# Performance work log

Measured on AMD Instinct MI355X. Metric: run time of the kernel, lower is better.

The kernel has to match this reference:

```python
import jax, jax.numpy as jnp
import numpy as np


def _log_g(x):
    # log of g(x) = where(x>=0, x+0.5, sigmoid(x)), computed stably in log-space
    return jnp.where(x >= 0, jnp.log(jax.nn.relu(x) + 0.5), -jax.nn.softplus(-x))


def _mingru_layer(h, w_hg_l, w_out_l, rms_w_l):
    # h: [B,T,H]; w_hg_l: [2*DI,H]; w_out_l: [H,DI]; rms_w_l: [H]
    hg = jnp.einsum('bth,dh->btd', h, w_hg_l)          # [B,T,2*DI]
    hidden, gate = jnp.split(hg, 2, axis=-1)            # each [B,T,DI]
    log_coeffs = -jax.nn.softplus(gate)                 # log a_t
    log_values = -jax.nn.softplus(-gate) + _log_g(hidden)  # log(z_t * g(h~_t))
    # Heinsen log-space associative scan (prev_hidden = 0, contributes nothing)
    a_star = jnp.cumsum(log_coeffs, axis=1)
    log_h = a_star + jax.lax.cumlogsumexp(log_values - a_star, axis=1)
    out = jnp.exp(log_h)                                # [B,T,DI]
    out = jnp.einsum('btd,hd->bth', out, w_out_l) + h   # proj_out + residual
    eps = jnp.finfo(out.dtype).eps
    out = out * jax.lax.rsqrt(jnp.mean(out * out, axis=-1, keepdims=True) + eps)
    return out * rms_w_l


def setup_inputs() -> dict:
    key = jax.random.key(0)
    ks = jax.random.split(key, 6)
    B, T, OBS, H, DI, L, A = 32, 1024, 512, 512, 1024, 2, 16
    s = 0.05  # weight scale keeps softplus/exp chain well-conditioned
    return {
        'x': jax.random.normal(ks[0], (B, T, OBS), jnp.float32),
        'enc_w': s * jax.random.normal(ks[1], (H, OBS), jnp.float32),
        'enc_b': jnp.zeros((H,), jnp.float32),
        'w_hg': s * jax.random.normal(ks[2], (L, 2 * DI, H), jnp.float32),
        'w_out': s * jax.random.normal(ks[3], (L, H, DI), jnp.float32),
        'rms_w': jnp.ones((L, H), jnp.float32),
        'dec_w': s * jax.random.normal(ks[4], (A, H), jnp.float32),
        'dec_b': jnp.zeros((A,), jnp.float32),
        'val_w': s * jax.random.normal(ks[5], (1, H), jnp.float32),
        'val_b': jnp.zeros((1,), jnp.float32),
    }


def reference(x, enc_w, enc_b, w_hg, w_out, rms_w, dec_w, dec_b, val_w, val_b):
    B, T, _ = x.shape
    # encoder: Linear + exact gelu
    h = jax.nn.gelu(jnp.einsum('bto,ho->bth', x, enc_w) + enc_b, approximate=False)
    for l in range(w_hg.shape[0]):
        h = _mingru_layer(h, w_hg[l], w_out[l], rms_w[l])
    flat = h.reshape(B * T, -1)
    logits = flat @ dec_w.T + dec_b                     # [B*T, A]
    values = (flat @ val_w.T + val_b).reshape(B, T)
    return logits, values
```

## Files before the change

kernel.cpp:

```cpp
#include <hip/hip_runtime.h>
#include <math.h>

#define MROWS 32768
#define T_LEN 1024

typedef __attribute__((ext_vector_type(8))) short bf16x8;
typedef __attribute__((ext_vector_type(4))) float f32x4;

__device__ __forceinline__ unsigned short f2bf(float f) {
  union { float f; unsigned u; } x; x.f = f;
  unsigned r = x.u + 0x7fffu + ((x.u >> 16) & 1u);
  return (unsigned short)(r >> 16);
}
__device__ __forceinline__ float bf2f(unsigned short u) {
  union { unsigned u; float f; } x; x.u = ((unsigned)u) << 16; return x.f;
}

__device__ __forceinline__ void gload_lds16(const void* g, void* l) {
  __builtin_amdgcn_global_load_lds(
      (const __attribute__((address_space(1))) void*)g,
      (__attribute__((address_space(3))) void*)l, 16, 0, 0);
}

template<int MODE>
__global__ __launch_bounds__(256, 2)
void gemm_bt(const unsigned short* __restrict__ A, int lda,
             const unsigned short* __restrict__ B,
             int N, int K,
             const float* __restrict__ bias,
             const unsigned short* res,
             unsigned short* outb)
{
  __shared__ __align__(16) unsigned short sA[128 * 64];
  __shared__ __align__(16) unsigned short sB[128 * 64];
  const int tid  = threadIdx.x;
  const int wave = tid >> 6, lane = tid & 63;
  const int m0 = blockIdx.x * 128, n0 = blockIdx.y * 128;
  const int srow   = lane >> 3;
  const int sslotb = ((lane & 7) ^ srow) * 16;
  const int wm = wave & 1, wn = wave >> 1;
  const int r16 = lane & 15, q = lane >> 4;

  f32x4 acc[4][4];
#pragma unroll
  for (int i = 0; i < 4; i++)
#pragma unroll
    for (int j = 0; j < 4; j++)
#pragma unroll
      for (int e = 0; e < 4; e++) acc[i][j][e] = 0.0f;

  const char* Ab = (const char*)A;
  const char* Bb = (const char*)B;
  char* sAb = (char*)sA;
  char* sBb = (char*)sB;

  for (int kt = 0; kt < K; kt += 64) {
#pragma unroll
    for (int i = 0; i < 4; i++) {
      const int j = wave * 4 + i;
      const int row = j * 8 + srow;
      gload_lds16(Ab + ((size_t)(m0 + row) * lda + kt) * 2 + sslotb, sAb + j * 1024);
      gload_lds16(Bb + ((size_t)(n0 + row) * K   + kt) * 2 + sslotb, sBb + j * 1024);
    }
    __syncthreads();
#pragma unroll
    for (int kh = 0; kh < 2; kh++) {
      bf16x8 af[4], bfr[4];
#pragma unroll
      for (int mt = 0; mt < 4; mt++) {
        const int row = wm * 64 + mt * 16 + r16;
        af[mt] = *(const bf16x8*)(sAb + row * 128 + ((((kh << 2) | q) ^ (row & 7)) * 16));
      }
#pragma unroll
      for (int nt = 0; nt < 4; nt++) {
        const int row = wn * 64 + nt * 16 + r16;
        bfr[nt] = *(const bf16x8*)(sBb + row * 128 + ((((kh << 2) | q) ^ (row & 7)) * 16));
      }
#pragma unroll
      for (int mt = 0; mt < 4; mt++)
#pragma unroll
        for (int nt = 0; nt < 4; nt++)
          acc[mt][nt] = __builtin_amdgcn_mfma_f32_16x16x32_bf16(af[mt], bfr[nt], acc[mt][nt], 0, 0, 0);
    }
    __syncthreads();
  }

#pragma unroll
  for (int mt = 0; mt < 4; mt++) {
#pragma unroll
    for (int nt = 0; nt < 4; nt++) {
#pragma unroll
      for (int r = 0; r < 4; r++) {
        const int m = m0 + wm * 64 + mt * 16 + q * 4 + r;
        const int n = n0 + wn * 64 + nt * 16 + r16;
        const size_t idx = (size_t)m * N + n;
        float v = acc[mt][nt][r];
        if (MODE == 0) {
          v += bias[n];
          v = 0.5f * v * (1.0f + erff(v * 0.70710678118654752f));
        } else if (MODE == 2) {
          v += bf2f(res[idx]);
        }
        outb[idx] = f2bf(v);
      }
    }
  }
}

__global__ __launch_bounds__(1024)
void scan_kernel(unsigned short* hg) {
  __shared__ float sA[32 * 64];
  __shared__ float sH[32 * 64];
  __shared__ float sC[32 * 64];
  const int b  = blockIdx.x >> 4;
  const int dg = blockIdx.x & 15;
  const int tid = threadIdx.x;
  const int c  = tid >> 5;
  const int dl = tid & 31;
  unsigned int* base = (unsigned int*)(hg + (size_t)b * T_LEN * 2048);
  const int du = dg * 32 + dl;

  float A0 = 1.0f, A1 = 1.0f, h0 = 0.0f, h1 = 0.0f;
#pragma unroll 8
  for (int tl = 0; tl < 32; ++tl) {
    const int t = c * 32 + tl;
    const unsigned hidp = base[t * 1024 + du];
    const unsigned gtp  = base[t * 1024 + 512 + du];
    const float hid0 = bf2f((unsigned short)hidp), hid1 = bf2f((unsigned short)(hidp >> 16));
    const float gt0  = bf2f((unsigned short)gtp),  gt1  = bf2f((unsigned short)(gtp >> 16));
    const float z0 = 1.0f / (1.0f + __expf(-gt0));
    const float z1 = 1.0f / (1.0f + __expf(-gt1));
    const float g0 = (hid0 >= 0.0f) ? (hid0 + 0.5f) : (1.0f / (1.0f + __expf(-hid0)));
    const float g1 = (hid1 >= 0.0f) ? (hid1 + 0.5f) : (1.0f / (1.0f + __expf(-hid1)));
    const unsigned short ra0 = f2bf(1.0f - z0), rb0 = f2bf(z0 * g0);
    const unsigned short ra1 = f2bf(1.0f - z1), rb1 = f2bf(z1 * g1);
    base[t * 1024 + du]       = (unsigned)ra0 | ((unsigned)ra1 << 16);
    base[t * 1024 + 512 + du] = (unsigned)rb0 | ((unsigned)rb1 << 16);
    const float fa0 = bf2f(ra0), fb0 = bf2f(rb0), fa1 = bf2f(ra1), fb1 = bf2f(rb1);
    A0 *= fa0; h0 = fa0 * h0 + fb0;
    A1 *= fa1; h1 = fa1 * h1 + fb1;
  }
  sA[c * 64 + 2 * dl] = A0;  sA[c * 64 + 2 * dl + 1] = A1;
  sH[c * 64 + 2 * dl] = h0;  sH[c * 64 + 2 * dl + 1] = h1;
  __syncthreads();

  if (tid < 64) {
    float hin = 0.0f;
#pragma unroll
    for (int cc = 0; cc < 32; ++cc) {
      sC[cc * 64 + tid] = hin;
      hin = sH[cc * 64 + tid] + sA[cc * 64 + tid] * hin;
    }
  }
  __syncthreads();

  float hh0 = sC[c * 64 + 2 * dl];
  float hh1 = sC[c * 64 + 2 * dl + 1];
#pragma unroll 8
  for (int tl = 0; tl < 32; ++tl) {
    const int t = c * 32 + tl;
    const unsigned pa = base[t * 1024 + du];
    const unsigned pb = base[t * 1024 + 512 + du];
    const float fa0 = bf2f((unsigned short)pa), fa1 = bf2f((unsigned short)(pa >> 16));
    const float fb0 = bf2f((unsigned short)pb), fb1 = bf2f((unsigned short)(pb >> 16));
    hh0 = fa0 * hh0 + fb0;
    hh1 = fa1 * hh1 + fb1;
    base[t * 1024 + 512 + du] = (unsigned)f2bf(hh0) | ((unsigned)f2bf(hh1) << 16);
  }
}

__global__ __launch_bounds__(256)
void rms_kernel(unsigned short* __restrict__ hb, const float* __restrict__ w) {
  const int wid  = (blockIdx.x * blockDim.x + threadIdx.x) >> 6;
  const int lane = threadIdx.x & 63;
  unsigned short* row = hb + (size_t)wid * 512;
  float v[8];
  float ss = 0.0f;
#pragma unroll
  for (int j = 0; j < 8; j++) { v[j] = bf2f(row[lane + 64 * j]); ss += v[j] * v[j]; }
#pragma unroll
  for (int off = 32; off >= 1; off >>= 1) ss += __shfl_xor(ss, off, 64);
  const float r = rsqrtf(ss * (1.0f / 512.0f) + 1.1920929e-7f);
#pragma unroll
  for (int j = 0; j < 8; j++) {
    const int k = lane + 64 * j;
    row[k] = f2bf(v[j] * r * w[k]);
  }
}

__global__ __launch_bounds__(256)
void decoder_kernel(const unsigned short* __restrict__ hb,
                    const float* __restrict__ dec_w,
                    const float* __restrict__ dec_b,
                    const float* __restrict__ val_w,
                    const float* __restrict__ val_b,
                    float* __restrict__ out) {
  const int nw   = (gridDim.x * blockDim.x) >> 6;
  const int wid  = (blockIdx.x * blockDim.x + threadIdx.x) >> 6;
  const int lane = threadIdx.x & 63;
  float* logits = out;
  float* values = out + (size_t)MROWS * 16;
  for (int row = wid; row < MROWS; row += nw) {
    const unsigned short* hr = hb + (size_t)row * 512;
    float acc[17];
#pragma unroll
    for (int a = 0; a < 17; a++) acc[a] = 0.0f;
#pragma unroll
    for (int j = 0; j < 8; j++) {
      const int k = lane + 64 * j;
      const float hv = bf2f(hr[k]);
#pragma unroll
      for (int a = 0; a < 16; a++) acc[a] += hv * dec_w[a * 512 + k];
      acc[16] += hv * val_w[k];
    }
#pragma unroll
    for (int a = 0; a < 17; a++) {
#pragma unroll
      for (int off = 32; off >= 1; off >>= 1) acc[a] += __shfl_xor(acc[a], off, 64);
    }
    if (lane == 0) {
#pragma unroll
      for (int a = 0; a < 16; a++) logits[(size_t)row * 16 + a] = acc[a] + dec_b[a];
      values[row] = acc[16] + val_b[0];
    }
  }
}

__global__ __launch_bounds__(256)
void conv_bf16(const float* __restrict__ in, unsigned short* __restrict__ out, int n4) {
  const int i = blockIdx.x * blockDim.x + threadIdx.x;
  if (i < n4) {
    const float4 v = ((const float4*)in)[i];
    const unsigned long long pack =
        (unsigned long long)f2bf(v.x) |
        ((unsigned long long)f2bf(v.y) << 16) |
        ((unsigned long long)f2bf(v.z) << 32) |
        ((unsigned long long)f2bf(v.w) << 48);
    ((unsigned long long*)out)[i] = pack;
  }
}

extern "C" void kernel_launch(void* const* d_in, const int* in_sizes, int n_in,
                              void* d_out, int out_size, void* d_ws, size_t ws_size,
                              hipStream_t stream) {
  const float* x     = (const float*)d_in[0];
  const float* enc_w = (const float*)d_in[1];
  const float* enc_b = (const float*)d_in[2];
  const float* w_hg  = (const float*)d_in[3];
  const float* w_out = (const float*)d_in[4];
  const float* rms_w = (const float*)d_in[5];
  const float* dec_w = (const float*)d_in[6];
  const float* dec_b = (const float*)d_in[7];
  const float* val_w = (const float*)d_in[8];
  const float* val_b = (const float*)d_in[9];
  float* out = (float*)d_out;

  if (ws_size < 174587904u) return;

  char* ws = (char*)d_ws;
  unsigned short* hg   = (unsigned short*)(ws);
  unsigned short* xb   = (unsigned short*)(ws);
  unsigned short* hb   = (unsigned short*)(ws + 134217728);
  unsigned short* wenc = (unsigned short*)(ws + 167772160);
  unsigned short* whg  = wenc + 262144;
  unsigned short* wout = whg + 2097152;

  conv_bf16<<<16384, 256, 0, stream>>>(x, xb, 4194304);
  conv_bf16<<<256,   256, 0, stream>>>(enc_w, wenc, 65536);
  conv_bf16<<<2048,  256, 0, stream>>>(w_hg, whg, 524288);
  conv_bf16<<<1024,  256, 0, stream>>>(w_out, wout, 262144);

  gemm_bt<0><<<dim3(256, 4), 256, 0, stream>>>(xb, 512, wenc, 512, 512, enc_b, nullptr, hb);

  for (int l = 0; l < 2; ++l) {
    gemm_bt<1><<<dim3(256, 16), 256, 0, stream>>>(hb, 512, whg + (size_t)l * 1048576, 2048, 512,
                                                  nullptr, nullptr, hg);
    scan_kernel<<<512, 1024, 0, stream>>>(hg);
    gemm_bt<2><<<dim3(256, 4), 256, 0, stream>>>(hg + 1024, 2048, wout + (size_t)l * 524288,
                                                 512, 1024, nullptr, hb, hb);
    rms_kernel<<<8192, 256, 0, stream>>>(hb, rms_w + (size_t)l * 512);
  }

  decoder_kernel<<<512, 256, 0, stream>>>(hb, dec_w, dec_b, val_w, val_b, out);
}
```

Measured before the change: 659.0 us.

## Fuse gate/hidden activations into hg GEMM epilogue via interleaved weight rows

Weight rows of w_hg are interleaved so each hidden/gate pair lands in adjacent output columns of the GEMM. The epilogue then uses a lane shuffle to compute z*g and 1-z directly and writes them as b and a coefficients. The scan kernel no longer computes the sigmoids or rewrites its input in the first pass, which removes a read-modify-write of the 128MB hg buffer. The trade-off is a heavier GEMM epilogue with divergent stores and a scan output that now overwrites the b slot.

After: 762.3 us. +15.7%, slower.

```diff
diff --git a/kernel.cpp b/kernel.cpp
--- a/kernel.cpp
+++ b/kernel.cpp
@@ -93,15 +93,27 @@
       for (int r = 0; r < 4; r++) {
         const int m = m0 + wm * 64 + mt * 16 + q * 4 + r;
         const int n = n0 + wn * 64 + nt * 16 + r16;
-        const size_t idx = (size_t)m * N + n;
         float v = acc[mt][nt][r];
-        if (MODE == 0) {
-          v += bias[n];
-          v = 0.5f * v * (1.0f + erff(v * 0.70710678118654752f));
-        } else if (MODE == 2) {
-          v += bf2f(res[idx]);
+        if (MODE == 3) {
+          const float vp = __shfl_xor(v, 1);
+          const int d = n >> 1;
+          if ((n & 1) == 0) {
+            const float z = 1.0f / (1.0f + __expf(-vp));
+            const float g = (v >= 0.0f) ? (v + 0.5f) : (1.0f / (1.0f + __expf(-v)));
+            outb[(size_t)m * 2048 + d] = f2bf(z * g);
+          } else {
+            outb[(size_t)m * 2048 + 1024 + d] = f2bf(1.0f / (1.0f + __expf(v)));
+          }
+        } else {
+          const size_t idx = (size_t)m * N + n;
+          if (MODE == 0) {
+            v += bias[n];
+            v = 0.5f * v * (1.0f + erff(v * 0.70710678118654752f));
+          } else if (MODE == 2) {
+            v += bf2f(res[idx]);
+          }
+          outb[idx] = f2bf(v);
         }
-        outb[idx] = f2bf(v);
       }
     }
   }
@@ -124,19 +136,10 @@
 #pragma unroll 8
   for (int tl = 0; tl < 32; ++tl) {
     const int t = c * 32 + tl;
-    const unsigned hidp = base[t * 1024 + du];
-    const unsigned gtp  = base[t * 1024 + 512 + du];
-    const float hid0 = bf2f((unsigned short)hidp), hid1 = bf2f((unsigned short)(hidp >> 16));
-    const float gt0  = bf2f((unsigned short)gtp),  gt1  = bf2f((unsigned short)(gtp >> 16));
-    const float z0 = 1.0f / (1.0f + __expf(-gt0));
-    const float z1 = 1.0f / (1.0f + __expf(-gt1));
-    const float g0 = (hid0 >= 0.0f) ? (hid0 + 0.5f) : (1.0f / (1.0f + __expf(-hid0)));
-    const float g1 = (hid1 >= 0.0f) ? (hid1 + 0.5f) : (1.0f / (1.0f + __expf(-hid1)));
-    const unsigned short ra0 = f2bf(1.0f - z0), rb0 = f2bf(z0 * g0);
-    const unsigned short ra1 = f2bf(1.0f - z1), rb1 = f2bf(z1 * g1);
-    base[t * 1024 + du]       = (unsigned)ra0 | ((unsigned)ra1 << 16);
-    base[t * 1024 + 512 + du] = (unsigned)rb0 | ((unsigned)rb1 << 16);
-    const float fa0 = bf2f(ra0), fb0 = bf2f(rb0), fa1 = bf2f(ra1), fb1 = bf2f(rb1);
+    const unsigned pb = base[t * 1024 + du];
+    const unsigned pa = base[t * 1024 + 512 + du];
+    const float fa0 = bf2f((unsigned short)pa), fa1 = bf2f((unsigned short)(pa >> 16));
+    const float fb0 = bf2f((unsigned short)pb), fb1 = bf2f((unsigned short)(pb >> 16));
     A0 *= fa0; h0 = fa0 * h0 + fb0;
     A1 *= fa1; h1 = fa1 * h1 + fb1;
   }
@@ -159,13 +162,13 @@
 #pragma unroll 8
   for (int tl = 0; tl < 32; ++tl) {
     const int t = c * 32 + tl;
-    const unsigned pa = base[t * 1024 + du];
-    const unsigned pb = base[t * 1024 + 512 + du];
+    const unsigned pb = base[t * 1024 + du];
+    const unsigned pa = base[t * 1024 + 512 + du];
     const float fa0 = bf2f((unsigned short)pa), fa1 = bf2f((unsigned short)(pa >> 16));
     const float fb0 = bf2f((unsigned short)pb), fb1 = bf2f((unsigned short)(pb >> 16));
     hh0 = fa0 * hh0 + fb0;
     hh1 = fa1 * hh1 + fb1;
-    base[t * 1024 + 512 + du] = (unsigned)f2bf(hh0) | ((unsigned)f2bf(hh1) << 16);
+    base[t * 1024 + du] = (unsigned)f2bf(hh0) | ((unsigned)f2bf(hh1) << 16);
   }
 }
 
@@ -240,6 +243,23 @@
   }
 }
 
+__global__ __launch_bounds__(256)
+void conv_whg(const float* __restrict__ in, unsigned short* __restrict__ out) {
+  const int i = blockIdx.x * blockDim.x + threadIdx.x;
+  const int col4 = i & 127;
+  const int row  = i >> 7;
+  const int l    = row >> 11;
+  const int n    = row & 2047;
+  const int src  = (n & 1) ? (1024 + (n >> 1)) : (n >> 1);
+  const float4 v = ((const float4*)in)[(size_t)((l << 11) + src) * 128 + col4];
+  const unsigned long long pack =
+      (unsigned long long)f2bf(v.x) |
+      ((unsigned long long)f2bf(v.y) << 16) |
+      ((unsigned long long)f2bf(v.z) << 32) |
+      ((unsigned long long)f2bf(v.w) << 48);
+  ((unsigned long long*)out)[i] = pack;
+}
+
 extern "C" void kernel_launch(void* const* d_in, const int* in_sizes, int n_in,
                               void* d_out, int out_size, void* d_ws, size_t ws_size,
                               hipStream_t stream) {
@@ -267,16 +287,16 @@
 
   conv_bf16<<<16384, 256, 0, stream>>>(x, xb, 4194304);
   conv_bf16<<<256,   256, 0, stream>>>(enc_w, wenc, 65536);
-  conv_bf16<<<2048,  256, 0, stream>>>(w_hg, whg, 524288);
+  conv_whg <<<2048,  256, 0, stream>>>(w_hg, whg);
   conv_bf16<<<1024,  256, 0, stream>>>(w_out, wout, 262144);
 
   gemm_bt<0><<<dim3(256, 4), 256, 0, stream>>>(xb, 512, wenc, 512, 512, enc_b, nullptr, hb);
 
   for (int l = 0; l < 2; ++l) {
-    gemm_bt<1><<<dim3(256, 16), 256, 0, stream>>>(hb, 512, whg + (size_t)l * 1048576, 2048, 512,
+    gemm_bt<3><<<dim3(256, 16), 256, 0, stream>>>(hb, 512, whg + (size_t)l * 1048576, 2048, 512,
                                                   nullptr, nullptr, hg);
     scan_kernel<<<512, 1024, 0, stream>>>(hg);
-    gemm_bt<2><<<dim3(256, 4), 256, 0, stream>>>(hg + 1024, 2048, wout + (size_t)l * 524288,
+    gemm_bt<2><<<dim3(256, 4), 256, 0, stream>>>(hg, 2048, wout + (size_t)l * 524288,
                                                  512, 1024, nullptr, hb, hb);
     rms_kernel<<<8192, 256, 0, stream>>>(hb, rms_w + (size_t)l * 512);
   }
```

## Keep scan coefficients in registers and split scan into more chunks per block

Applied to the files above, without the earlier changes.

The scan kernel now holds the per-timestep (a, b) coefficient pairs in registers instead of writing them to global memory and reading them back in the second pass. That removes one global write and one global read of the coefficient pairs per element. The chunk count doubles to 64 chunks of 16 timesteps with 16 pairs per block, and the grid doubles to 1024 blocks for more parallelism. The coefficient 1-z is computed as e*r to reuse the exponential. The cost is higher register pressure from the 32 held values and a longer serial cross-chunk combine over 64 chunks.

After: 654.1 us. Within noise of the previous version (-0.7%).

```diff
diff --git a/kernel.cpp b/kernel.cpp
--- a/kernel.cpp
+++ b/kernel.cpp
@@ -109,60 +109,59 @@
 
 __global__ __launch_bounds__(1024)
 void scan_kernel(unsigned short* hg) {
-  __shared__ float sA[32 * 64];
-  __shared__ float sH[32 * 64];
-  __shared__ float sC[32 * 64];
-  const int b  = blockIdx.x >> 4;
-  const int dg = blockIdx.x & 15;
+  __shared__ float sA[64 * 32];
+  __shared__ float sH[64 * 32];
+  __shared__ float sC[64 * 32];
+  const int b  = blockIdx.x >> 5;
+  const int dg = blockIdx.x & 31;
   const int tid = threadIdx.x;
-  const int c  = tid >> 5;
-  const int dl = tid & 31;
+  const int c  = tid >> 4;
+  const int dp = tid & 15;
   unsigned int* base = (unsigned int*)(hg + (size_t)b * T_LEN * 2048);
-  const int du = dg * 32 + dl;
-
+  const int du = dg * 16 + dp;
+
+  unsigned int pa[16], pb[16];
   float A0 = 1.0f, A1 = 1.0f, h0 = 0.0f, h1 = 0.0f;
-#pragma unroll 8
-  for (int tl = 0; tl < 32; ++tl) {
-    const int t = c * 32 + tl;
+#pragma unroll
+  for (int tl = 0; tl < 16; ++tl) {
+    const int t = c * 16 + tl;
     const unsigned hidp = base[t * 1024 + du];
     const unsigned gtp  = base[t * 1024 + 512 + du];
     const float hid0 = bf2f((unsigned short)hidp), hid1 = bf2f((unsigned short)(hidp >> 16));
     const float gt0  = bf2f((unsigned short)gtp),  gt1  = bf2f((unsigned short)(gtp >> 16));
-    const float z0 = 1.0f / (1.0f + __expf(-gt0));
-    const float z1 = 1.0f / (1.0f + __expf(-gt1));
+    const float e0 = __expf(-gt0), e1 = __expf(-gt1);
+    const float r0 = 1.0f / (1.0f + e0), r1 = 1.0f / (1.0f + e1);
     const float g0 = (hid0 >= 0.0f) ? (hid0 + 0.5f) : (1.0f / (1.0f + __expf(-hid0)));
     const float g1 = (hid1 >= 0.0f) ? (hid1 + 0.5f) : (1.0f / (1.0f + __expf(-hid1)));
-    const unsigned short ra0 = f2bf(1.0f - z0), rb0 = f2bf(z0 * g0);
-    const unsigned short ra1 = f2bf(1.0f - z1), rb1 = f2bf(z1 * g1);
-    base[t * 1024 + du]       = (unsigned)ra0 | ((unsigned)ra1 << 16);
-    base[t * 1024 + 512 + du] = (unsigned)rb0 | ((unsigned)rb1 << 16);
+    const unsigned short ra0 = f2bf(e0 * r0), rb0 = f2bf(r0 * g0);
+    const unsigned short ra1 = f2bf(e1 * r1), rb1 = f2bf(r1 * g1);
+    pa[tl] = (unsigned)ra0 | ((unsigned)ra1 << 16);
+    pb[tl] = (unsigned)rb0 | ((unsigned)rb1 << 16);
     const float fa0 = bf2f(ra0), fb0 = bf2f(rb0), fa1 = bf2f(ra1), fb1 = bf2f(rb1);
     A0 *= fa0; h0 = fa0 * h0 + fb0;
     A1 *= fa1; h1 = fa1 * h1 + fb1;
   }
-  sA[c * 64 + 2 * dl] = A0;  sA[c * 64 + 2 * dl + 1] = A1;
-  sH[c * 64 + 2 * dl] = h0;  sH[c * 64 + 2 * dl + 1] = h1;
+  sA[c * 32 + 2 * dp] = A0;  sA[c * 32 + 2 * dp + 1] = A1;
+  sH[c * 32 + 2 * dp] = h0;  sH[c * 32 + 2 * dp + 1] = h1;
   __syncthreads();
 
-  if (tid < 64) {
+  if (tid < 32) {
     float hin = 0.0f;
 #pragma unroll
-    for (int cc = 0; cc < 32; ++cc) {
-      sC[cc * 64 + tid] = hin;
-      hin = sH[cc * 64 + tid] + sA[cc * 64 + tid] * hin;
+    for (int cc = 0; cc < 64; ++cc) {
+      sC[cc * 32 + tid] = hin;
+      hin = sH[cc * 32 + tid] + sA[cc * 32 + tid] * hin;
     }
   }
   __syncthreads();
 
-  float hh0 = sC[c * 64 + 2 * dl];
-  float hh1 = sC[c * 64 + 2 * dl + 1];
-#pragma unroll 8
-  for (int tl = 0; tl < 32; ++tl) {
-    const int t = c * 32 + tl;
-    const unsigned pa = base[t * 1024 + du];
-    const unsigned pb = base[t * 1024 + 512 + du];
-    const float fa0 = bf2f((unsigned short)pa), fa1 = bf2f((unsigned short)(pa >> 16));
-    const float fb0 = bf2f((unsigned short)pb), fb1 = bf2f((unsigned short)(pb >> 16));
+  float hh0 = sC[c * 32 + 2 * dp];
+  float hh1 = sC[c * 32 + 2 * dp + 1];
+#pragma unroll
+  for (int tl = 0; tl < 16; ++tl) {
+    const int t = c * 16 + tl;
+    const float fa0 = bf2f((unsigned short)pa[tl]), fa1 = bf2f((unsigned short)(pa[tl] >> 16));
+    const float fb0 = bf2f((unsigned short)pb[tl]), fb1 = bf2f((unsigned short)(pb[tl] >> 16));
     hh0 = fa0 * hh0 + fb0;
     hh1 = fa1 * hh1 + fb1;
     base[t * 1024 + 512 + du] = (unsigned)f2bf(hh0) | ((unsigned)f2bf(hh1) << 16);
@@ -275,7 +274,7 @@
   for (int l = 0; l < 2; ++l) {
     gemm_bt<1><<<dim3(256, 16), 256, 0, stream>>>(hb, 512, whg + (size_t)l * 1048576, 2048, 512,
                                                   nullptr, nullptr, hg);
-    scan_kernel<<<512, 1024, 0, stream>>>(hg);
+    scan_kernel<<<1024, 1024, 0, stream>>>(hg);
     gemm_bt<2><<<dim3(256, 4), 256, 0, stream>>>(hg + 1024, 2048, wout + (size_t)l * 524288,
                                                  512, 1024, nullptr, hb, hb);
     rms_kernel<<<8192, 256, 0, stream>>>(hb, rms_w + (size_t)l * 512);
```
